# Kernel optimization log

Measured on AMD Instinct MI355X. Metric: run time of the kernel, lower is better.

## Reference

```python
import jax, jax.numpy as jnp
import numpy as np

EMBED = 768
HEAD = 128

def setup_inputs() -> dict:
    key = jax.random.key(0)
    ks = jax.random.split(key, 8)
    B, S = 8, 2048
    x = jax.random.normal(ks[0], (B, S, EMBED), dtype=jnp.float32)
    enc_output = jax.random.normal(ks[1], (B, S, EMBED), dtype=jnp.float32)
    s = 1.0 / np.sqrt(EMBED)
    Wq = jax.random.normal(ks[2], (EMBED, HEAD), dtype=jnp.float32) * s
    Wk = jax.random.normal(ks[3], (EMBED, HEAD), dtype=jnp.float32) * s
    Wv = jax.random.normal(ks[4], (EMBED, HEAD), dtype=jnp.float32) * s
    bq = jnp.zeros((HEAD,), dtype=jnp.float32)
    bk = jnp.zeros((HEAD,), dtype=jnp.float32)
    bv = jnp.zeros((HEAD,), dtype=jnp.float32)
    return {"x": x, "enc_output": enc_output, "Wq": Wq, "bq": bq,
            "Wk": Wk, "bk": bk, "Wv": Wv, "bv": bv}

def reference(x, enc_output, Wq, bq, Wk, bk, Wv, bv):
    # Faithful to original: Q, K, V all from x (enc_output is unused in the
    # original forward); scale is embed_size ** 0.5; dropout never applied.
    q = jnp.einsum('nse,ed->nsd', x, Wq) + bq  # [B,S,H]
    k = jnp.einsum('nse,ed->nsd', x, Wk) + bk
    v = jnp.einsum('nse,ed->nsd', x, Wv) + bv
    energy = jnp.einsum('nqd,nkd->nqk', q, k)  # [B,S,S]
    attn = jax.nn.softmax(energy / jnp.sqrt(jnp.float32(EMBED)), axis=2)
    out = jnp.einsum('nql,nld->nqd', attn, v)  # [B,S,H]
    return out
```

## Files before the change

### kernel.cpp

```cpp
#include <hip/hip_runtime.h>
#include <hip/hip_bf16.h>


typedef __bf16 bf16x8 __attribute__((ext_vector_type(8)));
typedef float f32x4 __attribute__((ext_vector_type(4)));
using bf16 = __hip_bfloat16;

#define EMB 768
#define HD 128
#define SEQ 2048
#define BATCH 8
#define ROWS (BATCH * SEQ)
#define NSPLIT 4
#define KVB 32
#define TILES_PER_SPLIT (SEQ / KVB / NSPLIT)

__global__ __launch_bounds__(256) void wt_kernel(
    const float* __restrict__ Wq, const float* __restrict__ Wk,
    const float* __restrict__ Wv, bf16* __restrict__ Wt)
{
    __shared__ float t_lds[32][33];
    const int tid = threadIdx.x;
    const int k0 = blockIdx.x * 32;
    const int n0 = blockIdx.y * 32;
    const int mtx = blockIdx.z;
    const float* W = (mtx == 0) ? Wq : (mtx == 1) ? Wk : Wv;
    const int j = tid & 31, i0 = tid >> 5;
#pragma unroll
    for (int c = 0; c < 4; ++c)
        t_lds[i0 + 8 * c][j] = W[(size_t)(k0 + i0 + 8 * c) * HD + n0 + j];
    __syncthreads();
#pragma unroll
    for (int c = 0; c < 4; ++c)
        Wt[(size_t)mtx * HD * EMB + (size_t)(n0 + i0 + 8 * c) * EMB + k0 + j] =
            __float2bfloat16(t_lds[j][i0 + 8 * c]);
}

__global__ __launch_bounds__(256, 3) void qkv_kernel(
    const float* __restrict__ x, const bf16* __restrict__ Wt,
    const float* __restrict__ bq, const float* __restrict__ bk,
    const float* __restrict__ bv,
    bf16* __restrict__ Q, bf16* __restrict__ K, bf16* __restrict__ Vt)
{
    __shared__ alignas(16) bf16 b_lds[2][128 * 64];
    const int tid  = threadIdx.x;
    const int sel  = blockIdx.y;
    const int row0 = blockIdx.x * 64;
    const int lane = tid & 63, wave = tid >> 6;
    const int lr = lane & 15, lq = lane >> 4;

    const char* Wb = (const char*)(Wt + (size_t)sel * HD * EMB);
    const int rl = lane >> 3;
    const int chlog = (lane & 7) ^ rl;

    const float* arow = &x[(size_t)(row0 + wave * 16 + lr) * EMB + lq * 8];

    float4 araw[2][2];
    auto loadA = [&](int kt) {
#pragma unroll
        for (int ks = 0; ks < 2; ++ks) {
            const float* p = arow + kt * 64 + ks * 32;
            araw[ks][0] = *reinterpret_cast<const float4*>(p);
            araw[ks][1] = *reinterpret_cast<const float4*>(p + 4);
        }
    };
    auto stageB = [&](int kt, int pb) {
#pragma unroll
        for (int c = 0; c < 4; ++c) {
            int r = c * 32 + wave * 8 + rl;
            const char* src = Wb + (size_t)r * (EMB * 2) + kt * 128 + chlog * 16;
            bf16* dst = &b_lds[pb][(size_t)(c * 32 + wave * 8) * 64];
            __builtin_amdgcn_global_load_lds(
                (const __attribute__((address_space(1))) void*)src,
                (__attribute__((address_space(3))) void*)dst, 16, 0, 0);
        }
    };

    f32x4 acc[8];
#pragma unroll
    for (int j = 0; j < 8; ++j) acc[j] = f32x4{0.f, 0.f, 0.f, 0.f};

    stageB(0, 0);
    loadA(0);
    __syncthreads();

    for (int kt = 0; kt < EMB / 64; ++kt) {
        const int p = kt & 1;
        if (kt < 11) stageB(kt + 1, p ^ 1);
        bf16x8 af[2];
#pragma unroll
        for (int ks = 0; ks < 2; ++ks) {
            union { bf16 h[8]; bf16x8 v; } u;
            u.h[0] = __float2bfloat16(araw[ks][0].x);
            u.h[1] = __float2bfloat16(araw[ks][0].y);
            u.h[2] = __float2bfloat16(araw[ks][0].z);
            u.h[3] = __float2bfloat16(araw[ks][0].w);
            u.h[4] = __float2bfloat16(araw[ks][1].x);
            u.h[5] = __float2bfloat16(araw[ks][1].y);
            u.h[6] = __float2bfloat16(araw[ks][1].z);
            u.h[7] = __float2bfloat16(araw[ks][1].w);
            af[ks] = u.v;
        }
        if (kt < 11) loadA(kt + 1);
#pragma unroll
        for (int ks = 0; ks < 2; ++ks)
#pragma unroll
            for (int nt = 0; nt < 8; ++nt) {
                const bf16x8 b = *reinterpret_cast<const bf16x8*>(
                    &b_lds[p][((nt * 16 + lr) * 8 + ((ks * 4 + lq) ^ (lr & 7))) * 8]);
                acc[nt] = __builtin_amdgcn_mfma_f32_16x16x32_bf16(af[ks], b, acc[nt], 0, 0, 0);
            }
        __syncthreads();
    }

    bf16 (*o_lds)[132] = reinterpret_cast<bf16(*)[132]>(&b_lds[0][0]);
    const float* bias = (sel == 0) ? bq : (sel == 1) ? bk : bv;
#pragma unroll
    for (int nt = 0; nt < 8; ++nt) {
        int col = nt * 16 + lr;
        float bb = bias[col];
#pragma unroll
        for (int rg = 0; rg < 4; ++rg)
            o_lds[wave * 16 + lq * 4 + rg][col] = __float2bfloat16(acc[nt][rg] + bb);
    }
    __syncthreads();
    if (sel < 2) {
        bf16* dst = (sel == 0) ? Q : K;
#pragma unroll
        for (int c = 0; c < 4; ++c) {
            int lin = tid + c * 256;
            int r = lin >> 4, ch = lin & 15;
            *reinterpret_cast<uint4*>(&dst[(size_t)(row0 + r) * HD + ch * 8]) =
                *reinterpret_cast<const uint4*>(&o_lds[r][ch * 8]);
        }
    } else {
        int d = tid >> 1, sh = (tid & 1) * 32;
        int bi = row0 >> 11, s0 = row0 & (SEQ - 1);
        union { bf16 h[32]; uint4 u4[4]; } pk;
#pragma unroll
        for (int s = 0; s < 32; ++s) pk.h[s] = o_lds[sh + s][d];
        bf16* base = &Vt[((size_t)bi * HD + d) * SEQ + s0 + sh];
#pragma unroll
        for (int c = 0; c < 4; ++c)
            *reinterpret_cast<uint4*>(base + c * 8) = pk.u4[c];
    }
}

__global__ __launch_bounds__(256, 2) void flash_kernel(
    const bf16* __restrict__ Q, const bf16* __restrict__ K,
    const bf16* __restrict__ Vt,
    float* __restrict__ Opart, float* __restrict__ Lpart)
{
    __shared__ alignas(16) bf16 k_lds[2][32][128];
    __shared__ alignas(16) bf16 v_lds[2][128][32];
    __shared__ alignas(16) bf16 p_lds[4][32][32];
    const int tid = threadIdx.x;
    const int lane = tid & 63, wave = tid >> 6;
    const int lr = lane & 15, lq = lane >> 4;
    const int b  = blockIdx.y;
    const int split = blockIdx.z;
    const int q0 = blockIdx.x * 128;
    const int qrow = b * SEQ + q0 + wave * 32;

    const float sc = 0.03608439182435161f * 1.44269504088896f;

    const int krl = lane >> 4, ksl = lane & 15;
    const int vrl = lane >> 2, vsl = lane & 3;

    auto stage = [&](int t, int pb) {
#pragma unroll
        for (int c = 0; c < 2; ++c) {
            int rbase = c * 16 + wave * 4;
            int r = rbase + krl;
            int ch = ksl ^ (r & 7);
            const bf16* src = &K[(size_t)(b * SEQ + t * KVB + r) * HD + ch * 8];
            bf16* dst = &k_lds[pb][rbase][0];
            __builtin_amdgcn_global_load_lds(
                (const __attribute__((address_space(1))) void*)src,
                (__attribute__((address_space(3))) void*)dst, 16, 0, 0);
        }
#pragma unroll
        for (int c = 0; c < 2; ++c) {
            int rbase = c * 64 + wave * 16;
            int r = rbase + vrl;
            int ch = vsl ^ ((r >> 1) & 3);
            const bf16* src = &Vt[((size_t)b * HD + r) * SEQ + t * KVB + ch * 8];
            bf16* dst = &v_lds[pb][rbase][0];
            __builtin_amdgcn_global_load_lds(
                (const __attribute__((address_space(1))) void*)src,
                (__attribute__((address_space(3))) void*)dst, 16, 0, 0);
        }
    };

    bf16x8 qf[2][4];
#pragma unroll
    for (int qt = 0; qt < 2; ++qt)
#pragma unroll
        for (int ks = 0; ks < 4; ++ks)
            qf[qt][ks] = *reinterpret_cast<const bf16x8*>(
                &Q[(size_t)(qrow + qt * 16 + lr) * HD + ks * 32 + lq * 8]);

    f32x4 o[2][8];
#pragma unroll
    for (int qt = 0; qt < 2; ++qt)
#pragma unroll
        for (int d = 0; d < 8; ++d) o[qt][d] = f32x4{0.f, 0.f, 0.f, 0.f};
    float lsum[2] = {0.f, 0.f};

    const int t0 = split * TILES_PER_SPLIT, t1 = t0 + TILES_PER_SPLIT;
    stage(t0, 0);
    __syncthreads();

    char* prow0 = (char*)&p_lds[wave][lr][0];
    char* prow1 = (char*)&p_lds[wave][16 + lr][0];
    const int psw = (lr >> 1) & 3;

    for (int t = t0; t < t1; ++t) {
        const int pb = (t - t0) & 1;
        if (t + 1 < t1) stage(t + 1, pb ^ 1);

#pragma unroll
        for (int nt = 0; nt < 2; ++nt) {
            bf16x8 kf[4];
#pragma unroll
            for (int ks = 0; ks < 4; ++ks)
                kf[ks] = *reinterpret_cast<const bf16x8*>(
                    &k_lds[pb][nt * 16 + lr][((ks * 4 + lq) ^ (lr & 7)) * 8]);
#pragma unroll
            for (int qt = 0; qt < 2; ++qt) {
                f32x4 s = f32x4{0.f, 0.f, 0.f, 0.f};
#pragma unroll
                for (int ks = 0; ks < 4; ++ks)
                    s = __builtin_amdgcn_mfma_f32_16x16x32_bf16(kf[ks], qf[qt][ks], s, 0, 0, 0);
                union { bf16 h[4]; uint2 u; } pk;
#pragma unroll
                for (int r = 0; r < 4; ++r) {
                    float e = exp2f(__builtin_fmaf(s[r], sc, -8.0f));
                    pk.h[r] = __float2bfloat16(e);
                    lsum[qt] += __bfloat162float(pk.h[r]);
                }
                char* prow = qt ? prow1 : prow0;
                *reinterpret_cast<uint2*>(
                    prow + (((nt * 2 + (lq >> 1)) ^ psw) << 4) + ((lq & 1) << 3)) = pk.u;
            }
        }

        bf16x8 pf[2];
#pragma unroll
        for (int qt = 0; qt < 2; ++qt) {
            const char* prow = qt ? prow1 : prow0;
            pf[qt] = *reinterpret_cast<const bf16x8*>(prow + ((lq ^ psw) << 4));
        }
#pragma unroll
        for (int d = 0; d < 8; ++d) {
            int vr = d * 16 + lr;
            bf16x8 vf = *reinterpret_cast<const bf16x8*>(
                &v_lds[pb][vr][(lq ^ ((vr >> 1) & 3)) * 8]);
#pragma unroll
            for (int qt = 0; qt < 2; ++qt)
                o[qt][d] = __builtin_amdgcn_mfma_f32_16x16x32_bf16(vf, pf[qt], o[qt][d], 0, 0, 0);
        }
        __syncthreads();
    }

#pragma unroll
    for (int qt = 0; qt < 2; ++qt) {
        lsum[qt] += __shfl_xor(lsum[qt], 16);
        lsum[qt] += __shfl_xor(lsum[qt], 32);
    }

    const size_t obase = (size_t)split * ROWS;
#pragma unroll
    for (int qt = 0; qt < 2; ++qt) {
#pragma unroll
        for (int d = 0; d < 8; ++d)
            *reinterpret_cast<f32x4*>(
                &Opart[(obase + qrow + qt * 16 + lr) * HD + d * 16 + lq * 4]) = o[qt][d];
        if (lane < 16)
            Lpart[obase + qrow + qt * 16 + lr] = lsum[qt];
    }
}

__global__ __launch_bounds__(256) void combine_kernel(
    const float* __restrict__ Opart, const float* __restrict__ Lpart,
    float* __restrict__ out)
{
    int gid = blockIdx.x * 256 + threadIdx.x;
    int row = gid >> 5, dc = gid & 31;
    float L = 0.f;
#pragma unroll
    for (int s = 0; s < NSPLIT; ++s)
        L += Lpart[(size_t)s * ROWS + row];
    float4 acc = {0.f, 0.f, 0.f, 0.f};
#pragma unroll
    for (int s = 0; s < NSPLIT; ++s) {
        float4 v = *reinterpret_cast<const float4*>(&Opart[((size_t)s * ROWS + row) * HD + dc * 4]);
        acc.x += v.x; acc.y += v.y; acc.z += v.z; acc.w += v.w;
    }
    float inv = 1.f / L;
    acc.x *= inv; acc.y *= inv; acc.z *= inv; acc.w *= inv;
    *reinterpret_cast<float4*>(&out[(size_t)row * HD + dc * 4]) = acc;
}

extern "C" void kernel_launch(void* const* d_in, const int* in_sizes, int n_in,
                              void* d_out, int out_size, void* d_ws, size_t ws_size,
                              hipStream_t stream) {
    const float* x  = (const float*)d_in[0];
    const float* Wq = (const float*)d_in[2];
    const float* bq = (const float*)d_in[3];
    const float* Wk = (const float*)d_in[4];
    const float* bk = (const float*)d_in[5];
    const float* Wv = (const float*)d_in[6];
    const float* bv = (const float*)d_in[7];
    float* out = (float*)d_out;

    char* ws = (char*)d_ws;
    const size_t WT_BYTES  = (size_t)3 * HD * EMB * 2;
    const size_t QKV_BYTES = (size_t)ROWS * HD * 2;
    const size_t OP_BYTES  = (size_t)NSPLIT * ROWS * HD * 4;
    bf16*  Wt    = (bf16*)ws;
    bf16*  Qb    = (bf16*)(ws + WT_BYTES);
    bf16*  Kb    = (bf16*)(ws + WT_BYTES + QKV_BYTES);
    bf16*  Vt    = (bf16*)(ws + WT_BYTES + 2 * QKV_BYTES);
    float* Opart = (float*)(ws + WT_BYTES + 3 * QKV_BYTES);
    float* Lpart = (float*)(ws + WT_BYTES + 3 * QKV_BYTES + OP_BYTES);

    hipLaunchKernelGGL(wt_kernel, dim3(EMB / 32, HD / 32, 3), dim3(256), 0, stream,
                       Wq, Wk, Wv, Wt);
    hipLaunchKernelGGL(qkv_kernel, dim3(ROWS / 64, 3), dim3(256), 0, stream,
                       x, Wt, bq, bk, bv, Qb, Kb, Vt);
    hipLaunchKernelGGL(flash_kernel, dim3(SEQ / 128, BATCH, NSPLIT), dim3(256), 0, stream,
                       Qb, Kb, Vt, Opart, Lpart);
    hipLaunchKernelGGL(combine_kernel, dim3(ROWS * 32 / 256), dim3(256), 0, stream,
                       Opart, Lpart, out);
}
```

Baseline: 185.7 us.

## Fuse split-KV combine into flash kernel via last-block atomic counter

Removes the separate combine kernel launch. Each flash block increments a per-query-tile counter after writing its partial output, and the last of the four splits sums the partials, normalizes, and writes the final output. The counters are zeroed inside the QKV kernel. This saves one launch and its tail, but adds atomics, fences, and a serialized reduction on the last-arriving block.

```diff
diff --git a/kernel.cpp b/kernel.cpp
--- a/kernel.cpp
+++ b/kernel.cpp
@@ -14,6 +14,7 @@
 #define NSPLIT 4
 #define KVB 32
 #define TILES_PER_SPLIT (SEQ / KVB / NSPLIT)
+#define NQT (SEQ / 128)
 
 __global__ __launch_bounds__(256) void wt_kernel(
     const float* __restrict__ Wq, const float* __restrict__ Wk,
@@ -40,7 +41,8 @@
     const float* __restrict__ x, const bf16* __restrict__ Wt,
     const float* __restrict__ bq, const float* __restrict__ bk,
     const float* __restrict__ bv,
-    bf16* __restrict__ Q, bf16* __restrict__ K, bf16* __restrict__ Vt)
+    bf16* __restrict__ Q, bf16* __restrict__ K, bf16* __restrict__ Vt,
+    int* __restrict__ cnt)
 {
     __shared__ alignas(16) bf16 b_lds[2][128 * 64];
     const int tid  = threadIdx.x;
@@ -48,6 +50,8 @@
     const int row0 = blockIdx.x * 64;
     const int lane = tid & 63, wave = tid >> 6;
     const int lr = lane & 15, lq = lane >> 4;
+
+    if (blockIdx.x == 0 && sel == 0 && tid < BATCH * NQT) cnt[tid] = 0;
 
     const char* Wb = (const char*)(Wt + (size_t)sel * HD * EMB);
     const int rl = lane >> 3;
@@ -149,11 +153,14 @@
 __global__ __launch_bounds__(256, 2) void flash_kernel(
     const bf16* __restrict__ Q, const bf16* __restrict__ K,
     const bf16* __restrict__ Vt,
-    float* __restrict__ Opart, float* __restrict__ Lpart)
+    float* __restrict__ Opart, float* __restrict__ Lpart,
+    int* __restrict__ cnt, float* __restrict__ out)
 {
     __shared__ alignas(16) bf16 k_lds[2][32][128];
     __shared__ alignas(16) bf16 v_lds[2][128][32];
     __shared__ alignas(16) bf16 p_lds[4][32][32];
+    __shared__ float linv[128];
+    __shared__ int s_old;
     const int tid = threadIdx.x;
     const int lane = tid & 63, wave = tid >> 6;
     const int lr = lane & 15, lq = lane >> 4;
@@ -279,27 +286,36 @@
         if (lane < 16)
             Lpart[obase + qrow + qt * 16 + lr] = lsum[qt];
     }
-}
-
-__global__ __launch_bounds__(256) void combine_kernel(
-    const float* __restrict__ Opart, const float* __restrict__ Lpart,
-    float* __restrict__ out)
-{
-    int gid = blockIdx.x * 256 + threadIdx.x;
-    int row = gid >> 5, dc = gid & 31;
-    float L = 0.f;
-#pragma unroll
-    for (int s = 0; s < NSPLIT; ++s)
-        L += Lpart[(size_t)s * ROWS + row];
-    float4 acc = {0.f, 0.f, 0.f, 0.f};
-#pragma unroll
-    for (int s = 0; s < NSPLIT; ++s) {
-        float4 v = *reinterpret_cast<const float4*>(&Opart[((size_t)s * ROWS + row) * HD + dc * 4]);
-        acc.x += v.x; acc.y += v.y; acc.z += v.z; acc.w += v.w;
-    }
-    float inv = 1.f / L;
-    acc.x *= inv; acc.y *= inv; acc.z *= inv; acc.w *= inv;
-    *reinterpret_cast<float4*>(&out[(size_t)row * HD + dc * 4]) = acc;
+
+    __threadfence();
+    if (tid == 0) s_old = atomicAdd(&cnt[b * NQT + blockIdx.x], 1);
+    __syncthreads();
+    if (s_old == 3) {
+        __threadfence();
+        const int rbase = b * SEQ + q0;
+        for (int r = tid; r < 128; r += 256) {
+            float L = 0.f;
+#pragma unroll
+            for (int s = 0; s < NSPLIT; ++s)
+                L += Lpart[(size_t)s * ROWS + rbase + r];
+            linv[r] = 1.f / L;
+        }
+        __syncthreads();
+        for (int u = tid; u < 128 * 32; u += 256) {
+            int r = u >> 5, c = u & 31;
+            size_t off = (size_t)(rbase + r) * HD + c * 4;
+            float4 a = {0.f, 0.f, 0.f, 0.f};
+#pragma unroll
+            for (int s = 0; s < NSPLIT; ++s) {
+                float4 v = *reinterpret_cast<const float4*>(
+                    &Opart[(size_t)s * ROWS * HD + off]);
+                a.x += v.x; a.y += v.y; a.z += v.z; a.w += v.w;
+            }
+            float iv = linv[r];
+            a.x *= iv; a.y *= iv; a.z *= iv; a.w *= iv;
+            *reinterpret_cast<float4*>(&out[off]) = a;
+        }
+    }
 }
 
 extern "C" void kernel_launch(void* const* d_in, const int* in_sizes, int n_in,
@@ -318,19 +334,19 @@
     const size_t WT_BYTES  = (size_t)3 * HD * EMB * 2;
     const size_t QKV_BYTES = (size_t)ROWS * HD * 2;
     const size_t OP_BYTES  = (size_t)NSPLIT * ROWS * HD * 4;
+    const size_t LP_BYTES  = (size_t)NSPLIT * ROWS * 4;
     bf16*  Wt    = (bf16*)ws;
     bf16*  Qb    = (bf16*)(ws + WT_BYTES);
     bf16*  Kb    = (bf16*)(ws + WT_BYTES + QKV_BYTES);
     bf16*  Vt    = (bf16*)(ws + WT_BYTES + 2 * QKV_BYTES);
     float* Opart = (float*)(ws + WT_BYTES + 3 * QKV_BYTES);
     float* Lpart = (float*)(ws + WT_BYTES + 3 * QKV_BYTES + OP_BYTES);
+    int*   cnt   = (int*)  (ws + WT_BYTES + 3 * QKV_BYTES + OP_BYTES + LP_BYTES);
 
     hipLaunchKernelGGL(wt_kernel, dim3(EMB / 32, HD / 32, 3), dim3(256), 0, stream,
                        Wq, Wk, Wv, Wt);
     hipLaunchKernelGGL(qkv_kernel, dim3(ROWS / 64, 3), dim3(256), 0, stream,
-                       x, Wt, bq, bk, bv, Qb, Kb, Vt);
-    hipLaunchKernelGGL(flash_kernel, dim3(SEQ / 128, BATCH, NSPLIT), dim3(256), 0, stream,
-                       Qb, Kb, Vt, Opart, Lpart);
-    hipLaunchKernelGGL(combine_kernel, dim3(ROWS * 32 / 256), dim3(256), 0, stream,
-                       Opart, Lpart, out);
+                       x, Wt, bq, bk, bv, Qb, Kb, Vt, cnt);
+    hipLaunchKernelGGL(flash_kernel, dim3(NQT, BATCH, NSPLIT), dim3(256), 0, stream,
+                       Qb, Kb, Vt, Opart, Lpart, cnt, out);
 }
```

After: 259.8 us. 1.4x slower.
